# Kernel tuning notes

Hardware: AMD Instinct MI355X
Metric: run time of the kernel (lower is better)

Reference implementation:

```python
import jax, jax.numpy as jnp
import numpy as np

B, S, H, R = 32, 1024, 768, 24
ATT_EPS = 1e10
LN_EPS = 1e-12


def setup_inputs() -> dict:
    key = jax.random.key(0)
    ks = jax.random.split(key, 20)
    sc = 0.02
    inp = {
        "relation": jax.random.randint(ks[0], (B, 1), 0, R),
        "last_hidden_size": jax.random.normal(ks[1], (B, S, H), dtype=jnp.float32),
        "sub_head": jax.random.randint(ks[2], (B, 1), 0, S),
        "sub_tail": jax.random.randint(ks[3], (B, 1), 0, S),
        "attention_mask": jnp.ones((B, S), dtype=jnp.float32),
        # learned parameters
        "rel_emb": jax.random.normal(ks[4], (R, H)) * sc,
        "W_rf": jax.random.normal(ks[5], (H, H)) * sc,
        "b_rf": jnp.zeros((H,), jnp.float32),
        "gamma": jnp.ones((H,), jnp.float32),
        "beta": jnp.zeros((H,), jnp.float32),
        "W_wd": jax.random.normal(ks[6], (H, 2 * H)) * sc,
        "W_bd": jax.random.normal(ks[7], (H, 2 * H)) * sc,
        "Wq": jax.random.normal(ks[8], (H, H)) * sc,
        "bq": jnp.zeros((H,), jnp.float32),
        "Wk": jax.random.normal(ks[9], (H, H)) * sc,
        "bk": jnp.zeros((H,), jnp.float32),
        "Wv": jax.random.normal(ks[10], (H, H)) * sc,
        "bv": jnp.zeros((H,), jnp.float32),
        "W_obj": jax.random.normal(ks[11], (1, H)) * sc,
        "b_obj": jnp.zeros((1,), jnp.float32),
    }
    return inp


def reference(relation, last_hidden_size, sub_head, sub_tail, attention_mask,
              rel_emb, W_rf, b_rf, gamma, beta, W_wd, W_bd,
              Wq, bq, Wk, bk, Wv, bv, W_obj, b_obj):
    # dropout layers are identity in eval mode
    # relation feature: embedding -> linear -> ReLU6   [B,1,H]
    rel_feature = jnp.clip(rel_emb[relation] @ W_rf.T + b_rf, 0.0, 6.0)
    # subject span features via gather                 [B,1,H]
    sh = jnp.take_along_axis(last_hidden_size, sub_head[:, :, None], axis=1)
    st = jnp.take_along_axis(last_hidden_size, sub_tail[:, :, None], axis=1)
    sub_feature = (sh + st) * 0.5
    cond = jnp.concatenate([rel_feature, sub_feature], axis=-1)  # [B,1,2H]

    # conditional layer norm: per-sample affine from condition
    weight = cond @ W_wd.T + gamma  # [B,1,H]
    bias = cond @ W_bd.T + beta     # [B,1,H]
    mean = jnp.mean(last_hidden_size, axis=-1, keepdims=True)
    ctr = last_hidden_size - mean
    var = jnp.mean(ctr * ctr, axis=-1, keepdims=True)
    x = ctr / jnp.sqrt(var + LN_EPS)
    x = x * weight + bias  # [B,S,H]

    # custom attention: ReLU-activated q/k/v, additive mask bias, residual
    q = jax.nn.relu(x @ Wq.T + bq)
    k = jax.nn.relu(x @ Wk.T + bk)
    v = jax.nn.relu(x @ Wv.T + bv)
    e = jnp.einsum('bsh,bth->bst', q, k)  # [B,S,S]
    e = e - ATT_EPS * (1.0 - attention_mask[:, None, :])
    a = jax.nn.softmax(e, axis=-1)
    hidden = jnp.einsum('bst,bth->bsh', a, v) + x  # residual

    pred_obj_head = jnp.squeeze(hidden @ W_obj.T + b_obj, axis=-1)  # [B,S]
    return pred_obj_head, hidden
```

## Files before the change

kernel.cpp:

```cpp
#include <hip/hip_runtime.h>

constexpr int NB  = 32;
constexpr int NS  = 1024;
constexpr int NH  = 768;
constexpr int NH2 = 1536;
constexpr int NQKV = 2304;
constexpr int NBS = NB * NS;

typedef __bf16 bf16x8 __attribute__((ext_vector_type(8)));
typedef float  f32x4  __attribute__((ext_vector_type(4)));
typedef unsigned short u16x8 __attribute__((ext_vector_type(8)));

__device__ __forceinline__ unsigned short f2bf(float f) {
  unsigned int u = __builtin_bit_cast(unsigned int, f);
  u += 0x7FFFu + ((u >> 16) & 1u);
  return (unsigned short)(u >> 16);
}
__device__ __forceinline__ float bf2f(unsigned short h) {
  return __builtin_bit_cast(float, ((unsigned int)h) << 16);
}

#define GLDS16(g, l)                                                         \
  __builtin_amdgcn_global_load_lds(                                          \
      (__attribute__((address_space(1))) void*)(g),                          \
      (__attribute__((address_space(3))) void*)(l), 16, 0, 0)

#define SBAR()    asm volatile("s_barrier" ::: "memory")
#define WAITVM0() asm volatile("s_waitcnt vmcnt(0)" ::: "memory")
#define LGKM0()                                                              \
  do {                                                                       \
    asm volatile("s_waitcnt lgkmcnt(0)" ::: "memory");                       \
    __builtin_amdgcn_sched_barrier(0);                                       \
  } while (0)

__launch_bounds__(256)
__global__ void cond_pre(const int* __restrict__ relation,
                         const float* __restrict__ h,
                         const int* __restrict__ subh,
                         const int* __restrict__ subt,
                         const float* __restrict__ rel_emb,
                         float* __restrict__ reT, float* __restrict__ condT) {
  const int b = blockIdx.x, t = threadIdx.x;
  const int r = relation[b], sh = subh[b], st = subt[b];
  for (int k = t; k < NH; k += 256) {
    reT[(size_t)k * NB + b] = rel_emb[(size_t)r * NH + k];
    condT[(size_t)(NH + k) * NB + b] =
        0.5f * (h[((size_t)b * NS + sh) * NH + k] +
                h[((size_t)b * NS + st) * NH + k]);
  }
}

__launch_bounds__(256)
__global__ void cond_rf(const float* __restrict__ W_rf,
                        const float* __restrict__ b_rf,
                        const float* __restrict__ reT,
                        float* __restrict__ condT) {
  const int t = threadIdx.x;
  const int b = t & 31, jl = t >> 5;
  const int j = blockIdx.x * 8 + jl;
  const float4* w4 = (const float4*)(W_rf + (size_t)j * NH);
  const float* rT = reT + b;
  float a0 = 0.f, a1 = 0.f;
  for (int k4 = 0; k4 < NH / 4; k4++) {
    float4 w = w4[k4];
    const float* c = rT + (size_t)(k4 * 4) * NB;
    a0 += w.x * c[0] + w.y * c[NB];
    a1 += w.z * c[2 * NB] + w.w * c[3 * NB];
  }
  float acc = a0 + a1 + b_rf[j];
  condT[(size_t)j * NB + b] = fminf(fmaxf(acc, 0.0f), 6.0f);
}

__launch_bounds__(256)
__global__ void cond_wb(const float* __restrict__ W_wd,
                        const float* __restrict__ W_bd,
                        const float* __restrict__ gamma,
                        const float* __restrict__ beta,
                        const float* __restrict__ condT,
                        float* __restrict__ wt, float* __restrict__ bs) {
  __shared__ float redW[128], redB[128];
  const int t = threadIdx.x;
  const int b = t & 31, jl = (t >> 5) & 3, ks = t >> 7;
  const int j = blockIdx.x * 4 + jl;
  const float4* ww = (const float4*)(W_wd + (size_t)j * NH2 + ks * NH);
  const float4* wb = (const float4*)(W_bd + (size_t)j * NH2 + ks * NH);
  const float* cT = condT + (size_t)ks * NH * NB + b;
  float aw0 = 0.f, aw1 = 0.f, ab0 = 0.f, ab1 = 0.f;
  for (int k4 = 0; k4 < NH / 4; k4++) {
    float4 w = ww[k4];
    float4 v = wb[k4];
    const float* c = cT + (size_t)(k4 * 4) * NB;
    float c0 = c[0], c1 = c[NB], c2 = c[2 * NB], c3 = c[3 * NB];
    aw0 += w.x * c0 + w.y * c1;
    aw1 += w.z * c2 + w.w * c3;
    ab0 += v.x * c0 + v.y * c1;
    ab1 += v.z * c2 + v.w * c3;
  }
  float aw = aw0 + aw1, ab = ab0 + ab1;
  if (ks == 1) {
    redW[t - 128] = aw;
    redB[t - 128] = ab;
  }
  __syncthreads();
  if (ks == 0) {
    aw += redW[t];
    ab += redB[t];
    wt[(size_t)b * NH + j] = aw + gamma[j];
    bs[(size_t)b * NH + j] = ab + beta[j];
  }
}

__launch_bounds__(64)
__global__ void ln_kernel(const float* __restrict__ h,
                          const float* __restrict__ wt,
                          const float* __restrict__ bs,
                          unsigned short* __restrict__ xbf) {
  const int row = blockIdx.x;
  const int b = row >> 10;
  const int lane = threadIdx.x;
  const float4* hr = (const float4*)(h + (size_t)row * NH);
  float4 v0 = hr[lane], v1 = hr[lane + 64], v2 = hr[lane + 128];
  float sum = 0.f, sq = 0.f;
  {
    sum += v0.x + v0.y + v0.z + v0.w;
    sq  += v0.x * v0.x + v0.y * v0.y + v0.z * v0.z + v0.w * v0.w;
    sum += v1.x + v1.y + v1.z + v1.w;
    sq  += v1.x * v1.x + v1.y * v1.y + v1.z * v1.z + v1.w * v1.w;
    sum += v2.x + v2.y + v2.z + v2.w;
    sq  += v2.x * v2.x + v2.y * v2.y + v2.z * v2.z + v2.w * v2.w;
  }
  for (int off = 32; off > 0; off >>= 1) {
    sum += __shfl_xor(sum, off, 64);
    sq  += __shfl_xor(sq, off, 64);
  }
  const float mean = sum * (1.0f / NH);
  const float var  = sq * (1.0f / NH) - mean * mean;
  const float rstd = rsqrtf(var + 1e-12f);
  const float4* wr = (const float4*)(wt + (size_t)b * NH);
  const float4* br = (const float4*)(bs + (size_t)b * NH);
  ushort4* xr = (ushort4*)(xbf + (size_t)row * NH);
#pragma unroll
  for (int i = 0; i < 3; i++) {
    float4 v = (i == 0) ? v0 : (i == 1) ? v1 : v2;
    float4 w = wr[lane + 64 * i];
    float4 bb = br[lane + 64 * i];
    ushort4 o;
    o.x = f2bf((v.x - mean) * rstd * w.x + bb.x);
    o.y = f2bf((v.y - mean) * rstd * w.y + bb.y);
    o.z = f2bf((v.z - mean) * rstd * w.z + bb.z);
    o.w = f2bf((v.w - mean) * rstd * w.w + bb.w);
    xr[lane + 64 * i] = o;
  }
}

__launch_bounds__(256)
__global__ void prep_w(const float* __restrict__ Wq, const float* __restrict__ bq,
                       const float* __restrict__ Wk, const float* __restrict__ bk,
                       const float* __restrict__ Wv, const float* __restrict__ bv,
                       unsigned short* __restrict__ Wcat, float* __restrict__ bcat) {
  const int row = blockIdx.x;
  const float* Wsrc;
  const float* bsrc;
  int r;
  if (row < NH) { Wsrc = Wq; bsrc = bq; r = row; }
  else if (row < NH2) { Wsrc = Wk; bsrc = bk; r = row - NH; }
  else { Wsrc = Wv; bsrc = bv; r = row - NH2; }
  for (int j = threadIdx.x; j < NH; j += 256)
    Wcat[(size_t)row * NH + j] = f2bf(Wsrc[(size_t)r * NH + j]);
  if (threadIdx.x == 0) bcat[row] = bsrc[r];
}

template <int OUT_BF16, int RELU, int HASBIAS, int RES>
__launch_bounds__(512, 2)
__global__ void gemm256(const unsigned short* __restrict__ A, long long sAz, int lda,
                        const unsigned short* __restrict__ Bm, long long sBz, int ldb,
                        void* __restrict__ C, long long sCz, int ldc,
                        const float* __restrict__ bias,
                        const unsigned short* __restrict__ Res, long long sRz, int ldr,
                        int K, int doswz) {
  extern __shared__ char lds[];
  const int t = threadIdx.x;
  const int z = blockIdx.z;
  int id = blockIdx.x + blockIdx.y * gridDim.x;
  if (doswz) {
    const int cpx = (gridDim.x * gridDim.y) >> 3;
    id = (id & 7) * cpx + (id >> 3);
  }
  const int tileN = (id % gridDim.x) * 256;
  const int tileM = (id / gridDim.x) * 256;
  const unsigned short* Ab = A + (size_t)z * sAz + (size_t)tileM * lda;
  const unsigned short* Bb = Bm + (size_t)z * sBz + (size_t)tileN * ldb;

  const int lane = t & 63;
  const int w = t >> 6;
  const int wm = w >> 2, wn = w & 3;
  const int lr = lane & 15, hi = lane >> 4;
  const int swz = (lane & 7) << 4;
  const int rb0 = (wn & 1) * 64;

  const int sr = t >> 3;
  const int scc = (t & 7) ^ (sr & 7);

#define STAGE4(Gb, ld, dst)                                                 \
  do {                                                                      \
    _Pragma("unroll") for (int hl_ = 0; hl_ < 4; hl_++) {                   \
      GLDS16((Gb) + (size_t)(hl_ * 64 + sr) * (ld) + scc * 8,               \
             (dst) + hl_ * 8192 + (size_t)t * 16);                          \
    }                                                                       \
  } while (0)

#define RD_A(m0)                                                            \
  do {                                                                      \
    _Pragma("unroll") for (int mm_ = 0; mm_ < 4; mm_++)                     \
      _Pragma("unroll") for (int ks_ = 0; ks_ < 2; ks_++)                   \
        aF[mm_][ks_] = *(const bf16x8*)(Ah + ((m0) * 16 + mm_ * 16 + lr) * 128 + \
                                        ((ks_ * 64 + hi * 16) ^ swz));      \
  } while (0)

#define RD_B(n0)                                                            \
  do {                                                                      \
    _Pragma("unroll") for (int nn_ = 0; nn_ < 2; nn_++)                     \
      _Pragma("unroll") for (int ks_ = 0; ks_ < 2; ks_++)                   \
        bF[nn_][ks_] = *(const bf16x8*)(Bh + (rb0 + (n0) * 16 + nn_ * 16 + lr) * 128 + \
                                        ((ks_ * 64 + hi * 16) ^ swz));      \
  } while (0)

#define MFMA_Q(m0, n0)                                                      \
  do {                                                                      \
    __builtin_amdgcn_s_setprio(1);                                          \
    _Pragma("unroll") for (int ks_ = 0; ks_ < 2; ks_++)                     \
      _Pragma("unroll") for (int mm_ = 0; mm_ < 4; mm_++)                   \
        _Pragma("unroll") for (int nn_ = 0; nn_ < 2; nn_++)                 \
          acc[(m0) + mm_][(n0) + nn_] = __builtin_amdgcn_mfma_f32_16x16x32_bf16( \
              aF[mm_][ks_], bF[nn_][ks_], acc[(m0) + mm_][(n0) + nn_], 0, 0, 0); \
    __builtin_amdgcn_s_setprio(0);                                          \
  } while (0)

  f32x4 acc[8][4];
#pragma unroll
  for (int m = 0; m < 8; m++)
#pragma unroll
    for (int n = 0; n < 4; n++) acc[m][n] = (f32x4)0.0f;

  const int NT = K >> 6;

  STAGE4(Ab, lda, lds);
  STAGE4(Bb, ldb, lds + 65536);
  WAITVM0();
  SBAR();

  for (int kt = 0; kt < NT; kt++) {
    const int bb = kt & 1;
    const char* Ah = lds + bb * 32768 + wm * 16384;
    const char* Bh = lds + 65536 + bb * 32768 + (wn >> 1) * 16384;
    const int stg = (kt + 1 < NT);
    bf16x8 aF[4][2], bF[2][2];

    RD_A(0);
    RD_B(0);
    if (stg) STAGE4(Ab + (size_t)(kt + 1) * 64, lda, lds + (bb ^ 1) * 32768);
    SBAR();
    LGKM0();
    MFMA_Q(0, 0);
    SBAR();

    RD_B(2);
    if (stg)
      STAGE4(Bb + (size_t)(kt + 1) * 64, ldb, lds + 65536 + (bb ^ 1) * 32768);
    SBAR();
    LGKM0();
    MFMA_Q(0, 2);
    SBAR();

    RD_A(4);
    SBAR();
    LGKM0();
    MFMA_Q(4, 2);
    SBAR();

    RD_B(0);
    SBAR();
    LGKM0();
    MFMA_Q(4, 0);
    if (stg) WAITVM0();
    SBAR();
  }

  const int row0 = tileM + wm * 128;
  const int col0 = tileN + wn * 64;
#pragma unroll
  for (int m = 0; m < 8; m++) {
    const int rowb = row0 + m * 16 + hi * 4;
#pragma unroll
    for (int n = 0; n < 4; n++) {
      const int col = col0 + n * 16 + lr;
      const float bv = HASBIAS ? bias[col] : 0.0f;
      f32x4 v = acc[m][n];
#pragma unroll
      for (int r = 0; r < 4; r++) {
        float x = v[r] + bv;
        if (RELU) x = fmaxf(x, 0.0f);
        if (RES)
          x += bf2f(Res[(size_t)z * sRz + (size_t)(rowb + r) * ldr + col]);
        if (OUT_BF16)
          ((unsigned short*)C)[(size_t)z * sCz + (size_t)(rowb + r) * ldc + col] =
              f2bf(x);
        else
          ((float*)C)[(size_t)z * sCz + (size_t)(rowb + r) * ldc + col] = x;
      }
    }
  }
#undef STAGE4
#undef RD_A
#undef RD_B
#undef MFMA_Q
}

__launch_bounds__(256)
__global__ void softmax_kernel(float* __restrict__ e,
                               const float* __restrict__ mask, int b0) {
  const int ri = blockIdx.x;
  const int lb = blockIdx.y;
  const int b = b0 + lb;
  float* row = e + ((size_t)lb * NS + ri) * NS;
  const int t = threadIdx.x;
  float4 v = ((const float4*)row)[t];
  float4 m = ((const float4*)(mask + (size_t)b * NS))[t];
  v.x -= 1e10f * (1.0f - m.x);
  v.y -= 1e10f * (1.0f - m.y);
  v.z -= 1e10f * (1.0f - m.z);
  v.w -= 1e10f * (1.0f - m.w);
  float mx = fmaxf(fmaxf(v.x, v.y), fmaxf(v.z, v.w));
  __shared__ float red[4];
  for (int off = 32; off > 0; off >>= 1) mx = fmaxf(mx, __shfl_xor(mx, off, 64));
  if ((t & 63) == 0) red[t >> 6] = mx;
  __syncthreads();
  mx = fmaxf(fmaxf(red[0], red[1]), fmaxf(red[2], red[3]));
  const float e0 = __expf(v.x - mx), e1 = __expf(v.y - mx);
  const float e2 = __expf(v.z - mx), e3 = __expf(v.w - mx);
  float sm = e0 + e1 + e2 + e3;
  __syncthreads();
  for (int off = 32; off > 0; off >>= 1) sm += __shfl_xor(sm, off, 64);
  if ((t & 63) == 0) red[t >> 6] = sm;
  __syncthreads();
  sm = red[0] + red[1] + red[2] + red[3];
  const float inv = 1.0f / sm;
  ushort4 o;
  o.x = f2bf(e0 * inv);
  o.y = f2bf(e1 * inv);
  o.z = f2bf(e2 * inv);
  o.w = f2bf(e3 * inv);
  ((ushort4*)row)[t] = o;
}

__launch_bounds__(256)
__global__ void transpose_v(const unsigned short* __restrict__ qkv,
                            unsigned short* __restrict__ vT) {
  const int b = blockIdx.z;
  const int s0 = blockIdx.x * 64;
  const int h0 = blockIdx.y * 64;
  __shared__ unsigned short tile[64][72];
  const int t = threadIdx.x;
  const int tx = t & 7, ty = t >> 3;
  const unsigned short* src = qkv + ((size_t)(b * NS + s0)) * NQKV + NH2 + h0;
#pragma unroll
  for (int i = 0; i < 2; i++) {
    const int s = ty + 32 * i;
    u16x8 vv = *(const u16x8*)(src + (size_t)s * NQKV + tx * 8);
#pragma unroll
    for (int j = 0; j < 8; j++) tile[s][tx * 8 + j] = vv[j];
  }
  __syncthreads();
  unsigned short* dst = vT + ((size_t)b * NH + h0) * NS + s0;
#pragma unroll
  for (int i = 0; i < 2; i++) {
    const int hh = ty + 32 * i;
    u16x8 o;
#pragma unroll
    for (int j = 0; j < 8; j++) o[j] = tile[tx * 8 + j][hh];
    *(u16x8*)(dst + (size_t)hh * NS + tx * 8) = o;
  }
}

__launch_bounds__(64)
__global__ void pred_kernel(const float* __restrict__ hidden,
                            const float* __restrict__ wobj,
                            const float* __restrict__ bobj,
                            float* __restrict__ pred) {
  const int row = blockIdx.x;
  const int lane = threadIdx.x;
  const float4* hr = (const float4*)(hidden + (size_t)row * NH);
  const float4* wr = (const float4*)wobj;
  float s = 0.f;
#pragma unroll
  for (int i = 0; i < 3; i++) {
    float4 a = hr[lane + 64 * i];
    float4 w = wr[lane + 64 * i];
    s += a.x * w.x + a.y * w.y + a.z * w.z + a.w * w.w;
  }
  for (int off = 32; off > 0; off >>= 1) s += __shfl_xor(s, off, 64);
  if (lane == 0) pred[row] = s + bobj[0];
}

extern "C" void kernel_launch(void* const* d_in, const int* in_sizes, int n_in,
                              void* d_out, int out_size, void* d_ws,
                              size_t ws_size, hipStream_t stream) {
  const int* relation   = (const int*)d_in[0];
  const float* lhs      = (const float*)d_in[1];
  const int* sub_head   = (const int*)d_in[2];
  const int* sub_tail   = (const int*)d_in[3];
  const float* att_mask = (const float*)d_in[4];
  const float* rel_emb  = (const float*)d_in[5];
  const float* W_rf     = (const float*)d_in[6];
  const float* b_rf     = (const float*)d_in[7];
  const float* gamma    = (const float*)d_in[8];
  const float* beta     = (const float*)d_in[9];
  const float* W_wd     = (const float*)d_in[10];
  const float* W_bd     = (const float*)d_in[11];
  const float* Wq       = (const float*)d_in[12];
  const float* bq       = (const float*)d_in[13];
  const float* Wk       = (const float*)d_in[14];
  const float* bk       = (const float*)d_in[15];
  const float* Wv       = (const float*)d_in[16];
  const float* bv       = (const float*)d_in[17];
  const float* W_obj    = (const float*)d_in[18];
  const float* b_obj    = (const float*)d_in[19];

  char* ws = (char*)d_ws;
  unsigned short* Wcat = (unsigned short*)(ws + 0);
  float* bcat  = (float*)(ws + 3538944);
  float* wt    = (float*)(ws + 3548160);
  float* bs    = (float*)(ws + 3646464);
  float* reT   = (float*)(ws + 3744768);
  float* condT = (float*)(ws + 3843072);
  unsigned short* xbf = (unsigned short*)(ws + 4039680);
  unsigned short* qkv = (unsigned short*)(ws + 54371328);
  unsigned short* vT  = (unsigned short*)(ws + 205366272);
  float* ebuf = (float*)(ws + 255697920);

  float* out_pred = (float*)d_out;
  float* out_hidden = out_pred + NBS;

  const size_t fixed = 255697920ull;
  size_t avail = ws_size > fixed ? ws_size - fixed : 0;
  int CB = 32;
  while (CB > 1 && (size_t)CB * (size_t)NS * NS * 4 > avail) CB >>= 1;

  prep_w<<<dim3(NQKV), dim3(256), 0, stream>>>(Wq, bq, Wk, bk, Wv, bv, Wcat, bcat);
  cond_pre<<<dim3(NB), dim3(256), 0, stream>>>(relation, lhs, sub_head, sub_tail,
                                               rel_emb, reT, condT);
  cond_rf<<<dim3(NH / 8), dim3(256), 0, stream>>>(W_rf, b_rf, reT, condT);
  cond_wb<<<dim3(NH / 4), dim3(256), 0, stream>>>(W_wd, W_bd, gamma, beta, condT,
                                                  wt, bs);
  ln_kernel<<<dim3(NBS), dim3(64), 0, stream>>>(lhs, wt, bs, xbf);

  gemm256<1, 1, 1, 0><<<dim3(NQKV / 256, NBS / 256, 1), dim3(512), 131072, stream>>>(
      xbf, 0, NH, Wcat, 0, NH, qkv, 0, NQKV, bcat, nullptr, 0, 0, NH, 1);

  transpose_v<<<dim3(NS / 64, NH / 64, NB), dim3(256), 0, stream>>>(qkv, vT);

  for (int b0 = 0; b0 < NB; b0 += CB) {
    gemm256<0, 0, 0, 0><<<dim3(NS / 256, NS / 256, CB), dim3(512), 131072, stream>>>(
        qkv + (size_t)b0 * NS * NQKV, (long long)NS * NQKV, NQKV,
        qkv + (size_t)b0 * NS * NQKV + NH, (long long)NS * NQKV, NQKV,
        ebuf, (long long)NS * NS, NS, nullptr, nullptr, 0, 0, NH, 0);
    softmax_kernel<<<dim3(NS, CB), dim3(256), 0, stream>>>(ebuf, att_mask, b0);
    gemm256<0, 0, 0, 1><<<dim3(NH / 256, NS / 256, CB), dim3(512), 131072, stream>>>(
        (const unsigned short*)ebuf, (long long)NS * 2048, 2048,
        vT + (size_t)b0 * NH * NS, (long long)NH * NS, NS,
        out_hidden + (size_t)b0 * NS * NH, (long long)NS * NH, NH, nullptr,
        xbf + (size_t)b0 * NS * NH, (long long)NS * NH, NH, NS, 0);
  }

  pred_kernel<<<dim3(NBS), dim3(64), 0, stream>>>(out_hidden, W_obj, b_obj,
                                                  out_pred);
}
```

Measured before the change: 503.5 us.

## Deepen GEMM pipeline to prefetch two K-tiles ahead with partial vmcnt waits

Reworks the 256x256 GEMM main loop so half-tile loads for k-tile kt+2 are issued into buffer regions as soon as they are consumed. The loop waits with vmcnt(6) instead of draining all loads, so global-to-LDS traffic overlaps more MFMA work. B fragments are now loaded once per k-step into a larger register set. XCD-aware block remapping is applied to all GEMM launches and handles grids not divisible by 8. The changes add register pressure and tighter ordering constraints on barriers and buffer reuse.

```diff
diff --git a/kernel.cpp b/kernel.cpp
--- a/kernel.cpp
+++ b/kernel.cpp
@@ -26,6 +26,7 @@
       (__attribute__((address_space(3))) void*)(l), 16, 0, 0)
 
 #define SBAR()    asm volatile("s_barrier" ::: "memory")
+#define WAITVM6() asm volatile("s_waitcnt vmcnt(6)" ::: "memory")
 #define WAITVM0() asm volatile("s_waitcnt vmcnt(0)" ::: "memory")
 #define LGKM0()                                                              \
   do {                                                                       \
@@ -177,14 +178,16 @@
                         void* __restrict__ C, long long sCz, int ldc,
                         const float* __restrict__ bias,
                         const unsigned short* __restrict__ Res, long long sRz, int ldr,
-                        int K, int doswz) {
+                        int K) {
   extern __shared__ char lds[];
   const int t = threadIdx.x;
   const int z = blockIdx.z;
   int id = blockIdx.x + blockIdx.y * gridDim.x;
-  if (doswz) {
-    const int cpx = (gridDim.x * gridDim.y) >> 3;
-    id = (id & 7) * cpx + (id >> 3);
+  {
+    const int nwg = gridDim.x * gridDim.y;
+    const int q = nwg >> 3, r = nwg & 7;
+    const int xcd = id & 7, lid = id >> 3;
+    id = (xcd < r ? xcd * (q + 1) : r * (q + 1) + (xcd - r) * q) + lid;
   }
   const int tileN = (id % gridDim.x) * 256;
   const int tileM = (id / gridDim.x) * 256;
@@ -195,44 +198,44 @@
   const int w = t >> 6;
   const int wm = w >> 2, wn = w & 3;
   const int lr = lane & 15, hi = lane >> 4;
-  const int swz = (lane & 7) << 4;
-  const int rb0 = (wn & 1) * 64;
+  const int swz = (lr & 7) << 4;
+  const int brow0 = (wn & 1) * 64;
 
   const int sr = t >> 3;
   const int scc = (t & 7) ^ (sr & 7);
 
-#define STAGE4(Gb, ld, dst)                                                 \
+#define STAGEH(Gb, ld, kc, dst)                                             \
   do {                                                                      \
-    _Pragma("unroll") for (int hl_ = 0; hl_ < 4; hl_++) {                   \
-      GLDS16((Gb) + (size_t)(hl_ * 64 + sr) * (ld) + scc * 8,               \
-             (dst) + hl_ * 8192 + (size_t)t * 16);                          \
-    }                                                                       \
+    GLDS16((Gb) + (size_t)sr * (ld) + (kc) + scc * 8, (dst) + (size_t)t * 16); \
+    GLDS16((Gb) + (size_t)(64 + sr) * (ld) + (kc) + scc * 8,                \
+           (dst) + 8192 + (size_t)t * 16);                                  \
   } while (0)
 
-#define RD_A(m0)                                                            \
+#define RD_BALL(Bh)                                                         \
+  do {                                                                      \
+    _Pragma("unroll") for (int nn_ = 0; nn_ < 4; nn_++)                     \
+      _Pragma("unroll") for (int ks_ = 0; ks_ < 2; ks_++)                   \
+        bF[nn_][ks_] = *(const bf16x8*)((Bh) + (brow0 + nn_ * 16 + lr) * 128 + \
+                                        ((ks_ * 64 + hi * 16) ^ swz));      \
+  } while (0)
+
+#define RD_AH(m0, Ah)                                                       \
   do {                                                                      \
     _Pragma("unroll") for (int mm_ = 0; mm_ < 4; mm_++)                     \
       _Pragma("unroll") for (int ks_ = 0; ks_ < 2; ks_++)                   \
-        aF[mm_][ks_] = *(const bf16x8*)(Ah + ((m0) * 16 + mm_ * 16 + lr) * 128 + \
+        aF[mm_][ks_] = *(const bf16x8*)((Ah) + (((m0) + mm_) * 16 + lr) * 128 + \
                                         ((ks_ * 64 + hi * 16) ^ swz));      \
   } while (0)
 
-#define RD_B(n0)                                                            \
-  do {                                                                      \
-    _Pragma("unroll") for (int nn_ = 0; nn_ < 2; nn_++)                     \
-      _Pragma("unroll") for (int ks_ = 0; ks_ < 2; ks_++)                   \
-        bF[nn_][ks_] = *(const bf16x8*)(Bh + (rb0 + (n0) * 16 + nn_ * 16 + lr) * 128 + \
-                                        ((ks_ * 64 + hi * 16) ^ swz));      \
-  } while (0)
-
-#define MFMA_Q(m0, n0)                                                      \
+#define MFMAQ(mb, nb)                                                       \
   do {                                                                      \
     __builtin_amdgcn_s_setprio(1);                                          \
     _Pragma("unroll") for (int ks_ = 0; ks_ < 2; ks_++)                     \
       _Pragma("unroll") for (int mm_ = 0; mm_ < 4; mm_++)                   \
         _Pragma("unroll") for (int nn_ = 0; nn_ < 2; nn_++)                 \
-          acc[(m0) + mm_][(n0) + nn_] = __builtin_amdgcn_mfma_f32_16x16x32_bf16( \
-              aF[mm_][ks_], bF[nn_][ks_], acc[(m0) + mm_][(n0) + nn_], 0, 0, 0); \
+          acc[(mb) + mm_][(nb) + nn_] = __builtin_amdgcn_mfma_f32_16x16x32_bf16( \
+              aF[mm_][ks_], bF[(nb) + nn_][ks_], acc[(mb) + mm_][(nb) + nn_], \
+              0, 0, 0);                                                     \
     __builtin_amdgcn_s_setprio(0);                                          \
   } while (0)
 
@@ -244,45 +247,52 @@
 
   const int NT = K >> 6;
 
-  STAGE4(Ab, lda, lds);
-  STAGE4(Bb, ldb, lds + 65536);
-  WAITVM0();
+  STAGEH(Bb, ldb, 0, lds + 65536);
+  STAGEH(Bb + (size_t)128 * ldb, ldb, 0, lds + 65536 + 16384);
+  STAGEH(Ab, lda, 0, lds);
+  STAGEH(Ab + (size_t)128 * lda, lda, 0, lds + 16384);
+  STAGEH(Bb, ldb, 64, lds + 65536 + 32768);
+  STAGEH(Bb + (size_t)128 * ldb, ldb, 64, lds + 65536 + 32768 + 16384);
+  STAGEH(Ab, lda, 64, lds + 32768);
+  WAITVM6();
   SBAR();
 
   for (int kt = 0; kt < NT; kt++) {
-    const int bb = kt & 1;
-    const char* Ah = lds + bb * 32768 + wm * 16384;
-    const char* Bh = lds + 65536 + bb * 32768 + (wn >> 1) * 16384;
-    const int stg = (kt + 1 < NT);
-    bf16x8 aF[4][2], bF[2][2];
-
-    RD_A(0);
-    RD_B(0);
-    if (stg) STAGE4(Ab + (size_t)(kt + 1) * 64, lda, lds + (bb ^ 1) * 32768);
+    const int bc = kt & 1;
+    const char* Ah = lds + bc * 32768 + wm * 16384;
+    const char* Bh = lds + 65536 + bc * 32768 + (wn >> 1) * 16384;
+    bf16x8 aF[4][2], bF[4][2];
+    RD_BALL(Bh);
+    RD_AH(0, Ah);
+    if (kt + 1 < NT)
+      STAGEH(Ab + (size_t)128 * lda, lda, (kt + 1) * 64,
+             lds + (bc ^ 1) * 32768 + 16384);
     SBAR();
     LGKM0();
-    MFMA_Q(0, 0);
-    SBAR();
-
-    RD_B(2);
-    if (stg)
-      STAGE4(Bb + (size_t)(kt + 1) * 64, ldb, lds + 65536 + (bb ^ 1) * 32768);
+    MFMAQ(0, 0);
+    SBAR();
+    if (kt + 2 < NT)
+      STAGEH(Bb, ldb, (kt + 2) * 64, lds + 65536 + bc * 32768);
+    SBAR();
+    MFMAQ(0, 2);
+    SBAR();
+    RD_AH(4, Ah);
+    if (kt + 2 < NT)
+      STAGEH(Bb + (size_t)128 * ldb, ldb, (kt + 2) * 64,
+             lds + 65536 + bc * 32768 + 16384);
     SBAR();
     LGKM0();
-    MFMA_Q(0, 2);
-    SBAR();
-
-    RD_A(4);
-    SBAR();
-    LGKM0();
-    MFMA_Q(4, 2);
-    SBAR();
-
-    RD_B(0);
-    SBAR();
-    LGKM0();
-    MFMA_Q(4, 0);
-    if (stg) WAITVM0();
+    MFMAQ(4, 2);
+    SBAR();
+    if (kt + 2 < NT)
+      STAGEH(Ab, lda, (kt + 2) * 64, lds + bc * 32768);
+    SBAR();
+    MFMAQ(4, 0);
+    if (kt + 2 < NT) {
+      WAITVM6();
+    } else if (kt + 1 < NT) {
+      WAITVM0();
+    }
     SBAR();
   }
 
@@ -310,10 +320,10 @@
       }
     }
   }
-#undef STAGE4
-#undef RD_A
-#undef RD_B
-#undef MFMA_Q
+#undef STAGEH
+#undef RD_BALL
+#undef RD_AH
+#undef MFMAQ
 }
 
 __launch_bounds__(256)
@@ -455,7 +465,7 @@
   ln_kernel<<<dim3(NBS), dim3(64), 0, stream>>>(lhs, wt, bs, xbf);
 
   gemm256<1, 1, 1, 0><<<dim3(NQKV / 256, NBS / 256, 1), dim3(512), 131072, stream>>>(
-      xbf, 0, NH, Wcat, 0, NH, qkv, 0, NQKV, bcat, nullptr, 0, 0, NH, 1);
+      xbf, 0, NH, Wcat, 0, NH, qkv, 0, NQKV, bcat, nullptr, 0, 0, NH);
 
   transpose_v<<<dim3(NS / 64, NH / 64, NB), dim3(256), 0, stream>>>(qkv, vT);
 
@@ -463,13 +473,13 @@
     gemm256<0, 0, 0, 0><<<dim3(NS / 256, NS / 256, CB), dim3(512), 131072, stream>>>(
         qkv + (size_t)b0 * NS * NQKV, (long long)NS * NQKV, NQKV,
         qkv + (size_t)b0 * NS * NQKV + NH, (long long)NS * NQKV, NQKV,
-        ebuf, (long long)NS * NS, NS, nullptr, nullptr, 0, 0, NH, 0);
+        ebuf, (long long)NS * NS, NS, nullptr, nullptr, 0, 0, NH);
     softmax_kernel<<<dim3(NS, CB), dim3(256), 0, stream>>>(ebuf, att_mask, b0);
     gemm256<0, 0, 0, 1><<<dim3(NH / 256, NS / 256, CB), dim3(512), 131072, stream>>>(
         (const unsigned short*)ebuf, (long long)NS * 2048, 2048,
         vT + (size_t)b0 * NH * NS, (long long)NH * NS, NS,
         out_hidden + (size_t)b0 * NS * NH, (long long)NS * NH, NH, nullptr,
-        xbf + (size_t)b0 * NS * NH, (long long)NS * NH, NH, NS, 0);
+        xbf + (size_t)b0 * NS * NH, (long long)NS * NH, NH, NS);
   }
 
   pred_kernel<<<dim3(NBS), dim3(64), 0, stream>>>(out_hidden, W_obj, b_obj,
```

New measurement: 494.4 us. Within noise of the previous version (-1.8%).
